# Kernel tuning notes

Measured on AMD Instinct MI355X. Metric: run time of the kernel, lower is better.

The kernel has to match this reference:

```python
import jax, jax.numpy as jnp
import numpy as np

SIGMA_V = 0.5
SIGMA_D = 3.0
C = 5  # number of lane-instance classes present in gt_seg


def setup_inputs() -> dict:
    key = jax.random.key(0)
    k1, k2 = jax.random.split(key)
    emb = jax.random.normal(k1, (8, 8, 1024, 1024), dtype=jnp.float32)
    gt_seg = jax.random.randint(k2, (8, 1024, 1024), 0, C, dtype=jnp.int32)
    return {"emb": emb, "gt_seg": gt_seg}


def _per_sample_loss(xb, sb):
    # xb: [N, D] pixel embeddings, sb: [N] int cluster ids in [0, C)
    counts = jax.ops.segment_sum(jnp.ones(sb.shape, xb.dtype), sb, num_segments=C)  # [C]
    sums = jax.ops.segment_sum(xb, sb, num_segments=C)                               # [C, D]
    means = sums / counts[:, None]                                                   # [C, D]
    # var loss: per cluster, Frobenius norm of residuals (matches torch .norm() over whole tensor)
    res = xb - means[sb]                                                             # [N, D]
    ss = jax.ops.segment_sum(jnp.sum(res * res, axis=-1), sb, num_segments=C)        # [C]
    var_loss = jnp.mean(jax.nn.relu(jnp.sqrt(ss) - SIGMA_V))
    # dist loss: hinge on pairwise cluster-mean distances, i != j, ordered pairs
    d2 = jnp.sum((means[:, None, :] - means[None, :, :]) ** 2, axis=-1)              # [C, C]
    eye = jnp.eye(C, dtype=d2.dtype)
    d = jnp.sqrt(d2 + eye)  # +eye keeps sqrt away from 0 on the diagonal
    hinge = jax.nn.relu(SIGMA_D - d) * (1.0 - eye)
    dist_loss = jnp.sum(hinge) / (C * (C - 1))
    return var_loss + dist_loss


def reference(emb, gt_seg):
    B, D, H, W = emb.shape
    x = emb.reshape(B, D, H * W).transpose(0, 2, 1)  # [B, N, D]
    seg = gt_seg.reshape(B, -1)                      # [B, N]
    per_sample = jax.vmap(_per_sample_loss)(x, seg)  # [B]
    return jnp.mean(per_sample)
```

## Files before the change

kernel.cpp:

```cpp
#include <hip/hip_runtime.h>

#define BATCH   8
#define DIM     8
#define NPIX    (1024 * 1024)
#define NCLS    5
#define SIGMA_V 0.5f
#define SIGMA_D 3.0f

#define PBLK 256
#define TPB  256
#define NWAVE (TPB / 64)

#define ACC50 (NCLS * 10)
#define WS_FLOATS (BATCH * ACC50)

__global__ void lanenet_init_ws(float* __restrict__ ws) {
    int t = blockIdx.x * blockDim.x + threadIdx.x;
    if (t < WS_FLOATS) ws[t] = 0.0f;
}

__device__ __forceinline__ float wave_sum(float v) {
    #pragma unroll
    for (int off = 32; off > 0; off >>= 1)
        v += __shfl_xor(v, off, 64);
    return v;
}

__global__ void lanenet_accum(const float* __restrict__ emb,
                              const int* __restrict__ seg,
                              float* __restrict__ ws) {
    const int b = blockIdx.y;
    const float* embB = emb + (size_t)b * DIM * NPIX;
    const int4* segB  = (const int4*)(seg + (size_t)b * NPIX);

    const int w    = threadIdx.x >> 6;
    const int lane = threadIdx.x & 63;

    const float4* e0 = (const float4*)(embB + (size_t)(2 * w)     * NPIX);
    const float4* e1 = (const float4*)(embB + (size_t)(2 * w + 1) * NPIX);

    float cnt[NCLS], sq[NCLS], sm0[NCLS], sm1[NCLS];
    #pragma unroll
    for (int c = 0; c < NCLS; ++c) {
        cnt[c] = 0.0f; sq[c] = 0.0f; sm0[c] = 0.0f; sm1[c] = 0.0f;
    }

    const int nG = NPIX / 4;
    const int stride = PBLK * 64;

    for (int g = blockIdx.x * 64 + lane; g < nG; g += stride) {
        const int4 s4 = segB[g];
        const float4 xa = e0[g];
        const float4 xb = e1[g];

        #pragma unroll
        for (int p = 0; p < 4; ++p) {
            const int s =
                (p == 0) ? s4.x : (p == 1) ? s4.y : (p == 2) ? s4.z : s4.w;
            const float av =
                (p == 0) ? xa.x : (p == 1) ? xa.y : (p == 2) ? xa.z : xa.w;
            const float bv =
                (p == 0) ? xb.x : (p == 1) ? xb.y : (p == 2) ? xb.z : xb.w;

            const float n2 = fmaf(av, av, bv * bv);

            #pragma unroll
            for (int c = 0; c < NCLS; ++c) {
                const float sel = (s == c) ? 1.0f : 0.0f;
                cnt[c] += sel;
                sq[c]  = fmaf(sel, n2, sq[c]);
                sm0[c] = fmaf(sel, av, sm0[c]);
                sm1[c] = fmaf(sel, bv, sm1[c]);
            }
        }
    }

    __shared__ float r_cnt[NCLS];
    __shared__ float r_sq[NWAVE][NCLS];
    __shared__ float r_sm[NCLS][DIM];

    #pragma unroll
    for (int c = 0; c < NCLS; ++c) {
        float v = wave_sum(sq[c]);
        if (lane == 0) r_sq[w][c] = v;
        v = wave_sum(sm0[c]);
        if (lane == 0) r_sm[c][2 * w] = v;
        v = wave_sum(sm1[c]);
        if (lane == 0) r_sm[c][2 * w + 1] = v;
        v = wave_sum(cnt[c]);
        if (lane == 0 && w == 0) r_cnt[c] = v;
    }
    __syncthreads();

    if (threadIdx.x < ACC50) {
        const int c = threadIdx.x / 10;
        const int k = threadIdx.x % 10;
        float v;
        if (k == 0)      v = r_cnt[c];
        else if (k == 1) v = r_sq[0][c] + r_sq[1][c] + r_sq[2][c] + r_sq[3][c];
        else             v = r_sm[c][k - 2];
        atomicAdd(&ws[(size_t)b * ACC50 + threadIdx.x], v);
    }
}

__global__ void lanenet_finalize(const float* __restrict__ ws,
                                 float* __restrict__ out) {
    __shared__ float lsamp[BATCH];
    const int t = threadIdx.x;
    if (t < BATCH) {
        const float* a = ws + (size_t)t * ACC50;
        float m[NCLS][DIM];
        float var = 0.0f;
        #pragma unroll
        for (int c = 0; c < NCLS; ++c) {
            const float c0 = fmaxf(a[c * 10 + 0], 1.0f);
            const float qq = a[c * 10 + 1];
            float s2 = 0.0f;
            #pragma unroll
            for (int d = 0; d < DIM; ++d) {
                const float s = a[c * 10 + 2 + d];
                m[c][d] = s / c0;
                s2 = fmaf(s, s, s2);
            }
            float ss = qq - s2 / c0;
            ss = fmaxf(ss, 0.0f);
            var += fmaxf(sqrtf(ss) - SIGMA_V, 0.0f);
        }
        var *= (1.0f / NCLS);

        float dist = 0.0f;
        #pragma unroll
        for (int i = 0; i < NCLS; ++i) {
            #pragma unroll
            for (int j = i + 1; j < NCLS; ++j) {
                float d2 = 0.0f;
                #pragma unroll
                for (int d = 0; d < DIM; ++d) {
                    const float df = m[i][d] - m[j][d];
                    d2 = fmaf(df, df, d2);
                }
                dist += 2.0f * fmaxf(SIGMA_D - sqrtf(d2), 0.0f);
            }
        }
        dist *= (1.0f / (NCLS * (NCLS - 1)));

        lsamp[t] = var + dist;
    }
    __syncthreads();
    if (t == 0) {
        float s = 0.0f;
        #pragma unroll
        for (int b = 0; b < BATCH; ++b) s += lsamp[b];
        out[0] = s * (1.0f / BATCH);
    }
}

extern "C" void kernel_launch(void* const* d_in, const int* in_sizes, int n_in,
                              void* d_out, int out_size, void* d_ws, size_t ws_size,
                              hipStream_t stream) {
    (void)in_sizes; (void)n_in; (void)out_size; (void)ws_size;
    const float* emb = (const float*)d_in[0];
    const int*   seg = (const int*)d_in[1];
    float* out = (float*)d_out;
    float* ws  = (float*)d_ws;

    lanenet_init_ws<<<1, 512, 0, stream>>>(ws);
    dim3 grid(PBLK, BATCH);
    lanenet_accum<<<grid, TPB, 0, stream>>>(emb, seg, ws);
    lanenet_finalize<<<1, 64, 0, stream>>>(ws, out);
}
```

Baseline: 387.1 us.

## Fuse finalize into accum via last-block ticket, prefetch loads, pack FMAs

Merges the finalize kernel into the accumulation kernel: each block bumps an atomic ticket, and the last block to finish computes the loss. This removes one kernel launch. The main loop now has a fixed trip count and loads the next iteration's data while the current one is processed (software prefetch). Per-class accumulators are packed into 2-wide vectors so the compiler can emit packed FMAs. The risks are a threadfence and atomic-counter serialization, plus extra registers for the prefetched values.

```diff
diff --git a/kernel.cpp b/kernel.cpp
--- a/kernel.cpp
+++ b/kernel.cpp
@@ -10,13 +10,18 @@
 #define PBLK 256
 #define TPB  256
 #define NWAVE (TPB / 64)
+#define NBLOCKS (PBLK * BATCH)
+#define NIT ((NPIX / 4) / (PBLK * 64))
 
 #define ACC50 (NCLS * 10)
 #define WS_FLOATS (BATCH * ACC50)
+#define WS_TOTAL  (WS_FLOATS + 4)
+
+typedef float v2f __attribute__((ext_vector_type(2)));
 
 __global__ void lanenet_init_ws(float* __restrict__ ws) {
     int t = blockIdx.x * blockDim.x + threadIdx.x;
-    if (t < WS_FLOATS) ws[t] = 0.0f;
+    if (t < WS_TOTAL) ws[t] = 0.0f;
 }
 
 __device__ __forceinline__ float wave_sum(float v) {
@@ -28,7 +33,8 @@
 
 __global__ void lanenet_accum(const float* __restrict__ emb,
                               const int* __restrict__ seg,
-                              float* __restrict__ ws) {
+                              float* ws,
+                              float* __restrict__ out) {
     const int b = blockIdx.y;
     const float* embB = emb + (size_t)b * DIM * NPIX;
     const int4* segB  = (const int4*)(seg + (size_t)b * NPIX);
@@ -39,41 +45,50 @@
     const float4* e0 = (const float4*)(embB + (size_t)(2 * w)     * NPIX);
     const float4* e1 = (const float4*)(embB + (size_t)(2 * w + 1) * NPIX);
 
-    float cnt[NCLS], sq[NCLS], sm0[NCLS], sm1[NCLS];
+    v2f cs[NCLS];
+    v2f sm[NCLS];
     #pragma unroll
     for (int c = 0; c < NCLS; ++c) {
-        cnt[c] = 0.0f; sq[c] = 0.0f; sm0[c] = 0.0f; sm1[c] = 0.0f;
+        cs[c] = (v2f){0.0f, 0.0f};
+        sm[c] = (v2f){0.0f, 0.0f};
     }
 
-    const int nG = NPIX / 4;
-    const int stride = PBLK * 64;
+    auto pix = [&](int s, float av, float bv) {
+        const float n2 = fmaf(av, av, bv * bv);
+        const v2f ab = (v2f){av, bv};
+        const v2f w1 = (v2f){1.0f, n2};
+        #pragma unroll
+        for (int c = 0; c < NCLS; ++c) {
+            const float sel = (s == c) ? 1.0f : 0.0f;
+            const v2f sv = (v2f){sel, sel};
+            cs[c] = __builtin_elementwise_fma(sv, w1, cs[c]);
+            sm[c] = __builtin_elementwise_fma(sv, ab, sm[c]);
+        }
+    };
 
-    for (int g = blockIdx.x * 64 + lane; g < nG; g += stride) {
-        const int4 s4 = segB[g];
-        const float4 xa = e0[g];
-        const float4 xb = e1[g];
+    int g = blockIdx.x * 64 + lane;
+    int4   s4 = segB[g];
+    float4 xa = e0[g];
+    float4 xb = e1[g];
 
-        #pragma unroll
-        for (int p = 0; p < 4; ++p) {
-            const int s =
-                (p == 0) ? s4.x : (p == 1) ? s4.y : (p == 2) ? s4.z : s4.w;
-            const float av =
-                (p == 0) ? xa.x : (p == 1) ? xa.y : (p == 2) ? xa.z : xa.w;
-            const float bv =
-                (p == 0) ? xb.x : (p == 1) ? xb.y : (p == 2) ? xb.z : xb.w;
+    #pragma unroll 1
+    for (int it = 0; it < NIT - 1; ++it) {
+        const int gn = g + PBLK * 64;
+        const int4   s4n = segB[gn];
+        const float4 xan = e0[gn];
+        const float4 xbn = e1[gn];
 
-            const float n2 = fmaf(av, av, bv * bv);
+        pix(s4.x, xa.x, xb.x);
+        pix(s4.y, xa.y, xb.y);
+        pix(s4.z, xa.z, xb.z);
+        pix(s4.w, xa.w, xb.w);
 
-            #pragma unroll
-            for (int c = 0; c < NCLS; ++c) {
-                const float sel = (s == c) ? 1.0f : 0.0f;
-                cnt[c] += sel;
-                sq[c]  = fmaf(sel, n2, sq[c]);
-                sm0[c] = fmaf(sel, av, sm0[c]);
-                sm1[c] = fmaf(sel, bv, sm1[c]);
-            }
-        }
+        s4 = s4n; xa = xan; xb = xbn; g = gn;
     }
+    pix(s4.x, xa.x, xb.x);
+    pix(s4.y, xa.y, xb.y);
+    pix(s4.z, xa.z, xb.z);
+    pix(s4.w, xa.w, xb.w);
 
     __shared__ float r_cnt[NCLS];
     __shared__ float r_sq[NWAVE][NCLS];
@@ -81,13 +96,13 @@
 
     #pragma unroll
     for (int c = 0; c < NCLS; ++c) {
-        float v = wave_sum(sq[c]);
+        float v = wave_sum(cs[c].y);
         if (lane == 0) r_sq[w][c] = v;
-        v = wave_sum(sm0[c]);
+        v = wave_sum(sm[c].x);
         if (lane == 0) r_sm[c][2 * w] = v;
-        v = wave_sum(sm1[c]);
+        v = wave_sum(sm[c].y);
         if (lane == 0) r_sm[c][2 * w + 1] = v;
-        v = wave_sum(cnt[c]);
+        v = wave_sum(cs[c].x);
         if (lane == 0 && w == 0) r_cnt[c] = v;
     }
     __syncthreads();
@@ -101,24 +116,36 @@
         else             v = r_sm[c][k - 2];
         atomicAdd(&ws[(size_t)b * ACC50 + threadIdx.x], v);
     }
-}
 
-__global__ void lanenet_finalize(const float* __restrict__ ws,
-                                 float* __restrict__ out) {
+    __threadfence();
+    __syncthreads();
+    __shared__ int amLast;
+    if (threadIdx.x == 0) {
+        unsigned* tick = (unsigned*)(ws + WS_FLOATS);
+        amLast = (atomicAdd(tick, 1u) == (unsigned)(NBLOCKS - 1));
+    }
+    __syncthreads();
+    if (!amLast) return;
+
+    __shared__ float a[WS_FLOATS];
+    for (int i = threadIdx.x; i < WS_FLOATS; i += TPB)
+        a[i] = atomicAdd(&ws[i], 0.0f);
+    __syncthreads();
+
     __shared__ float lsamp[BATCH];
     const int t = threadIdx.x;
     if (t < BATCH) {
-        const float* a = ws + (size_t)t * ACC50;
+        const float* ab = a + t * ACC50;
         float m[NCLS][DIM];
         float var = 0.0f;
         #pragma unroll
         for (int c = 0; c < NCLS; ++c) {
-            const float c0 = fmaxf(a[c * 10 + 0], 1.0f);
-            const float qq = a[c * 10 + 1];
+            const float c0 = fmaxf(ab[c * 10 + 0], 1.0f);
+            const float qq = ab[c * 10 + 1];
             float s2 = 0.0f;
             #pragma unroll
             for (int d = 0; d < DIM; ++d) {
-                const float s = a[c * 10 + 2 + d];
+                const float s = ab[c * 10 + 2 + d];
                 m[c][d] = s / c0;
                 s2 = fmaf(s, s, s2);
             }
@@ -150,7 +177,7 @@
     if (t == 0) {
         float s = 0.0f;
         #pragma unroll
-        for (int b = 0; b < BATCH; ++b) s += lsamp[b];
+        for (int bb = 0; bb < BATCH; ++bb) s += lsamp[bb];
         out[0] = s * (1.0f / BATCH);
     }
 }
@@ -166,6 +193,5 @@
 
     lanenet_init_ws<<<1, 512, 0, stream>>>(ws);
     dim3 grid(PBLK, BATCH);
-    lanenet_accum<<<grid, TPB, 0, stream>>>(emb, seg, ws);
-    lanenet_finalize<<<1, 64, 0, stream>>>(ws, out);
+    lanenet_accum<<<grid, TPB, 0, stream>>>(emb, seg, ws, out);
 }
```

New measurement: 706.8 us. 1.83x slower.
